# Kernel optimization log

Measured on AMD Instinct MI355X. Metric: run time of the kernel, lower is better.

## Reference

```python
import jax, jax.numpy as jnp
import numpy as np

MA_K = 2 * 125 + 1  # 251, moving-average kernel
MV_K = 4 * 125 + 1  # 501, moving-variance kernel
EPS = 1e-5


def _avg_pool1d(x, K):
    """PyTorch F.avg_pool1d(stride=1, padding=(K-1)//2, count_include_pad=True)
    computed in O(L) via prefix sums. x: (B, C, L) -> (B, C, L)."""
    pad = (K - 1) // 2
    xp = jnp.pad(x, ((0, 0), (0, 0), (pad, pad)))  # zero pad, length L+K-1
    c = jnp.pad(jnp.cumsum(xp, axis=-1), ((0, 0), (0, 0), (1, 0)))  # length L+K
    return (c[..., K:] - c[..., :-K]) / K  # divide by K always (count_include_pad)


def setup_inputs() -> dict:
    key = jax.random.key(0)
    x = jax.random.normal(key, (8192, 1, 3750), dtype=jnp.float32)
    return {"x": x}


def reference(x):
    # global z-norm per (batch, channel); torch.std is unbiased (ddof=1)
    x = (x - jnp.mean(x, axis=2, keepdims=True)) / (
        jnp.std(x, axis=2, keepdims=True, ddof=1) + EPS)
    # remove moving average (kernel 251)
    x = x - _avg_pool1d(x, MA_K)
    # rescale by moving std (kernel 501)
    x = x / (jnp.sqrt(_avg_pool1d(x * x, MV_K)) + EPS)
    return x
```

## Files before the change

### kernel.cpp

```cpp
#include <hip/hip_runtime.h>
#include <math.h>

namespace {

constexpr int L      = 3750;
constexpr int NPAIR  = L / 2;
constexpr int BLK    = 256;
constexpr int CH     = 15;
constexpr int NCHUNK = L / CH;
constexpr int NFULL  = NPAIR / BLK;
constexpr int NTAIL  = NPAIR - NFULL * BLK;
constexpr float EPS  = 1e-5f;

__device__ __forceinline__ float frcp(float x)  { return __builtin_amdgcn_rcpf(x); }
__device__ __forceinline__ float fsqrt(float x) { return __builtin_amdgcn_sqrtf(x); }
__device__ __forceinline__ float frsq(float x)  { return __builtin_amdgcn_rsqf(x); }

__global__ __launch_bounds__(BLK, 8)
void preproc_kernel(const float* __restrict__ in, float* __restrict__ out) {
    __shared__ __align__(16) float sp[L + 2];
    __shared__ float sred[8];

    const int tid  = threadIdx.x;
    const int lane = tid & 63;
    const int wave = tid >> 6;
    const size_t rowoff = (size_t)blockIdx.x * (size_t)L;
    const float* rin  = in  + rowoff;
    float*       rout = out + rowoff;

    const bool active = (tid < NCHUNK);
    const int  base   = tid * CH;
    const bool tl     = (tid < NTAIL);

    {
        const float2* rin2 = reinterpret_cast<const float2*>(rin);
        float2 v[NFULL + 1];
        #pragma unroll
        for (int k = 0; k < NFULL; ++k) v[k] = rin2[k * BLK + tid];
        if (tl) v[NFULL] = rin2[NFULL * BLK + tid];
        float2* sp2 = reinterpret_cast<float2*>(sp);
        #pragma unroll
        for (int k = 0; k < NFULL; ++k) sp2[k * BLK + tid] = v[k];
        if (tl) sp2[NFULL * BLK + tid] = v[NFULL];
    }
    __syncthreads();

    float y[CH];
    float cy = 0.f, cy2 = 0.f;
    if (active) {
        #pragma unroll
        for (int j = 0; j < CH; ++j) {
            const float v = sp[base + j];
            y[j] = v;
            cy  += v;
            cy2  = fmaf(v, v, cy2);
        }
    } else {
        #pragma unroll
        for (int j = 0; j < CH; ++j) y[j] = 0.f;
    }
    float iy = cy;
    #pragma unroll
    for (int d = 1; d < 64; d <<= 1) {
        const float u = __shfl_up(iy, (unsigned)d, 64);
        if (lane >= d) iy += u;
    }
    float t2 = cy2;
    #pragma unroll
    for (int d = 1; d < 64; d <<= 1) t2 += __shfl_xor(t2, d, 64);
    if (lane == 63) { sred[wave] = iy; sred[4 + wave] = t2; }
    __syncthreads();
    float woff = 0.f;
    #pragma unroll
    for (int w = 0; w < 4; ++w) if (w < wave) woff += sred[w];
    const float totY  = sred[0] + sred[1] + sred[2] + sred[3];
    const float totY2 = sred[4] + sred[5] + sred[6] + sred[7];
    const float mean  = totY * (1.f / (float)L);
    const float var   = (totY2 - totY * mean) * (1.f / (float)(L - 1));
    const float s     = fsqrt(var) + EPS;
    const float epsS  = EPS * s;

    {
        float run = woff + iy - cy;
        if (active) {
            #pragma unroll
            for (int j = 0; j < CH; ++j) { sp[base + j] = run; run += y[j]; }
            if (tid == NCHUNK - 1) sp[L] = run;
        }
    }
    __syncthreads();

    const float inv251 = 1.f / 251.f;
    float cu = 0.f;
    if (active) {
        if (tid >= 9 && tid <= 240) {
            #pragma unroll
            for (int j = 0; j < CH; ++j) {
                const int i = base + j;
                const float sumY = sp[i + 126] - sp[i - 125];
                const float u = fmaf(sumY, -inv251, y[j]);
                y[j] = u;
                cu   = fmaf(u, u, cu);
            }
        } else {
            #pragma unroll
            for (int j = 0; j < CH; ++j) {
                const int i  = base + j;
                const int lo = (i > 125) ? i - 125 : 0;
                const int hi = (i + 126 < L) ? i + 126 : L;
                const float sumY = sp[hi] - sp[lo];
                const float cnt  = (float)(hi - lo);
                float u = y[j] - mean * (1.f - cnt * inv251);
                u = fmaf(sumY, -inv251, u);
                y[j] = u;
                cu   = fmaf(u, u, cu);
            }
        }
    }
    float iu = cu;
    #pragma unroll
    for (int d = 1; d < 64; d <<= 1) {
        const float u = __shfl_up(iu, (unsigned)d, 64);
        if (lane >= d) iu += u;
    }
    if (lane == 63) sred[wave] = iu;
    __syncthreads();
    float woff2 = 0.f;
    #pragma unroll
    for (int w = 0; w < 4; ++w) if (w < wave) woff2 += sred[w];

    {
        float run = woff2 + iu - cu;
        if (active) {
            #pragma unroll
            for (int j = 0; j < CH; ++j) { sp[base + j] = run; run = fmaf(y[j], y[j], run); }
            if (tid == NCHUNK - 1) sp[L] = run;
        }
    }
    __syncthreads();

    const float inv501 = 1.f / 501.f;
    if (active) {
        if (tid >= 17 && tid <= 232) {
            #pragma unroll
            for (int j = 0; j < CH; ++j) {
                const int i = base + j;
                const float W = fmaxf((sp[i + 251] - sp[i - 250]) * inv501, 0.f);
                const float t = frsq(W);
                y[j] = y[j] * t * fmaf(-epsS, t, 1.f);
            }
        } else {
            #pragma unroll
            for (int j = 0; j < CH; ++j) {
                const int i  = base + j;
                const int lo = (i > 250) ? i - 250 : 0;
                const int hi = (i + 251 < L) ? i + 251 : L;
                const float W = fmaxf((sp[hi] - sp[lo]) * inv501, 0.f);
                const float t = frsq(W);
                y[j] = y[j] * t * fmaf(-epsS, t, 1.f);
            }
        }
    }
    __syncthreads();

    if (active) {
        #pragma unroll
        for (int j = 0; j < CH; ++j) sp[base + j] = y[j];
    }
    __syncthreads();

    {
        const float2* sp2 = reinterpret_cast<const float2*>(sp);
        float2* rout2 = reinterpret_cast<float2*>(rout);
        float2 v[NFULL + 1];
        #pragma unroll
        for (int k = 0; k < NFULL; ++k) v[k] = sp2[k * BLK + tid];
        if (tl) v[NFULL] = sp2[NFULL * BLK + tid];
        #pragma unroll
        for (int k = 0; k < NFULL; ++k) rout2[k * BLK + tid] = v[k];
        if (tl) rout2[NFULL * BLK + tid] = v[NFULL];
    }
}

}

extern "C" void kernel_launch(void* const* d_in, const int* in_sizes, int n_in,
                              void* d_out, int out_size, void* d_ws, size_t ws_size,
                              hipStream_t stream) {
    const float* x = (const float*)d_in[0];
    float* out = (float*)d_out;
    const int rows = in_sizes[0] / L;
    preproc_kernel<<<rows, BLK, 0, stream>>>(x, out);
}
```

Measured before the change: 44.61 us.

## Process two rows per block to amortize barriers and raise per-thread ILP

Each block now handles two rows at once, interleaving the scans, reductions and window passes for both rows between shared barriers. This halves the number of barriers and launches per row and gives each thread independent work to overlap latency. The cost is doubled LDS per block and more registers (launch bounds lowered from 8 to 5), which reduces how many blocks fit per CU, and it assumes an even row count.

```diff
diff --git a/kernel.cpp b/kernel.cpp
--- a/kernel.cpp
+++ b/kernel.cpp
@@ -6,6 +6,7 @@
 constexpr int L      = 3750;
 constexpr int NPAIR  = L / 2;
 constexpr int BLK    = 256;
+constexpr int ROWS   = 2;
 constexpr int CH     = 15;
 constexpr int NCHUNK = L / CH;
 constexpr int NFULL  = NPAIR / BLK;
@@ -16,169 +17,206 @@
 __device__ __forceinline__ float fsqrt(float x) { return __builtin_amdgcn_sqrtf(x); }
 __device__ __forceinline__ float frsq(float x)  { return __builtin_amdgcn_rsqf(x); }
 
-__global__ __launch_bounds__(BLK, 8)
+__global__ __launch_bounds__(BLK, 5)
 void preproc_kernel(const float* __restrict__ in, float* __restrict__ out) {
-    __shared__ __align__(16) float sp[L + 2];
-    __shared__ float sred[8];
+    __shared__ __align__(16) float sp[ROWS][L + 2];
+    __shared__ float sred[ROWS][8];
 
     const int tid  = threadIdx.x;
     const int lane = tid & 63;
     const int wave = tid >> 6;
-    const size_t rowoff = (size_t)blockIdx.x * (size_t)L;
-    const float* rin  = in  + rowoff;
-    float*       rout = out + rowoff;
+    const size_t row0 = (size_t)blockIdx.x * (size_t)ROWS;
 
     const bool active = (tid < NCHUNK);
     const int  base   = tid * CH;
     const bool tl     = (tid < NTAIL);
 
     {
-        const float2* rin2 = reinterpret_cast<const float2*>(rin);
-        float2 v[NFULL + 1];
-        #pragma unroll
-        for (int k = 0; k < NFULL; ++k) v[k] = rin2[k * BLK + tid];
-        if (tl) v[NFULL] = rin2[NFULL * BLK + tid];
-        float2* sp2 = reinterpret_cast<float2*>(sp);
-        #pragma unroll
-        for (int k = 0; k < NFULL; ++k) sp2[k * BLK + tid] = v[k];
-        if (tl) sp2[NFULL * BLK + tid] = v[NFULL];
-    }
-    __syncthreads();
-
-    float y[CH];
-    float cy = 0.f, cy2 = 0.f;
-    if (active) {
-        #pragma unroll
-        for (int j = 0; j < CH; ++j) {
-            const float v = sp[base + j];
-            y[j] = v;
-            cy  += v;
-            cy2  = fmaf(v, v, cy2);
-        }
-    } else {
-        #pragma unroll
-        for (int j = 0; j < CH; ++j) y[j] = 0.f;
-    }
-    float iy = cy;
-    #pragma unroll
-    for (int d = 1; d < 64; d <<= 1) {
-        const float u = __shfl_up(iy, (unsigned)d, 64);
-        if (lane >= d) iy += u;
-    }
-    float t2 = cy2;
-    #pragma unroll
-    for (int d = 1; d < 64; d <<= 1) t2 += __shfl_xor(t2, d, 64);
-    if (lane == 63) { sred[wave] = iy; sred[4 + wave] = t2; }
-    __syncthreads();
-    float woff = 0.f;
-    #pragma unroll
-    for (int w = 0; w < 4; ++w) if (w < wave) woff += sred[w];
-    const float totY  = sred[0] + sred[1] + sred[2] + sred[3];
-    const float totY2 = sred[4] + sred[5] + sred[6] + sred[7];
-    const float mean  = totY * (1.f / (float)L);
-    const float var   = (totY2 - totY * mean) * (1.f / (float)(L - 1));
-    const float s     = fsqrt(var) + EPS;
-    const float epsS  = EPS * s;
+        float2 v[ROWS][NFULL + 1];
+        #pragma unroll
+        for (int r = 0; r < ROWS; ++r) {
+            const float2* rin2 = reinterpret_cast<const float2*>(in + (row0 + r) * L);
+            #pragma unroll
+            for (int k = 0; k < NFULL; ++k) v[r][k] = rin2[k * BLK + tid];
+            if (tl) v[r][NFULL] = rin2[NFULL * BLK + tid];
+        }
+        #pragma unroll
+        for (int r = 0; r < ROWS; ++r) {
+            float2* sp2 = reinterpret_cast<float2*>(&sp[r][0]);
+            #pragma unroll
+            for (int k = 0; k < NFULL; ++k) sp2[k * BLK + tid] = v[r][k];
+            if (tl) sp2[NFULL * BLK + tid] = v[r][NFULL];
+        }
+    }
+    __syncthreads();
+
+    float y[ROWS][CH];
+    float cy[ROWS], iy[ROWS];
+    #pragma unroll
+    for (int r = 0; r < ROWS; ++r) {
+        float c = 0.f, c2 = 0.f;
+        if (active) {
+            #pragma unroll
+            for (int j = 0; j < CH; ++j) {
+                const float v = sp[r][base + j];
+                y[r][j] = v;
+                c  += v;
+                c2  = fmaf(v, v, c2);
+            }
+        } else {
+            #pragma unroll
+            for (int j = 0; j < CH; ++j) y[r][j] = 0.f;
+        }
+        float i1 = c;
+        #pragma unroll
+        for (int d = 1; d < 64; d <<= 1) {
+            const float u = __shfl_up(i1, (unsigned)d, 64);
+            if (lane >= d) i1 += u;
+        }
+        float t2 = c2;
+        #pragma unroll
+        for (int d = 1; d < 64; d <<= 1) t2 += __shfl_xor(t2, d, 64);
+        if (lane == 63) { sred[r][wave] = i1; sred[r][4 + wave] = t2; }
+        cy[r] = c; iy[r] = i1;
+    }
+    __syncthreads();
+
+    float mean[ROWS], epsS[ROWS], woff[ROWS];
+    #pragma unroll
+    for (int r = 0; r < ROWS; ++r) {
+        float wo = 0.f;
+        #pragma unroll
+        for (int w = 0; w < 4; ++w) if (w < wave) wo += sred[r][w];
+        woff[r] = wo;
+        const float totY  = sred[r][0] + sred[r][1] + sred[r][2] + sred[r][3];
+        const float totY2 = sred[r][4] + sred[r][5] + sred[r][6] + sred[r][7];
+        mean[r] = totY * (1.f / (float)L);
+        const float var = (totY2 - totY * mean[r]) * (1.f / (float)(L - 1));
+        const float s   = fsqrt(var) + EPS;
+        epsS[r] = EPS * s;
+    }
+
+    #pragma unroll
+    for (int r = 0; r < ROWS; ++r) {
+        if (active) {
+            float run = woff[r] + iy[r] - cy[r];
+            #pragma unroll
+            for (int j = 0; j < CH; ++j) { sp[r][base + j] = run; run += y[r][j]; }
+            if (tid == NCHUNK - 1) sp[r][L] = run;
+        }
+    }
+    __syncthreads();
+
+    const float inv251 = 1.f / 251.f;
+    float cu[ROWS], iu[ROWS];
+    #pragma unroll
+    for (int r = 0; r < ROWS; ++r) {
+        float c = 0.f;
+        if (active) {
+            if (tid >= 9 && tid <= 240) {
+                #pragma unroll
+                for (int j = 0; j < CH; ++j) {
+                    const int i = base + j;
+                    const float sumY = sp[r][i + 126] - sp[r][i - 125];
+                    const float u = fmaf(sumY, -inv251, y[r][j]);
+                    y[r][j] = u;
+                    c = fmaf(u, u, c);
+                }
+            } else {
+                #pragma unroll
+                for (int j = 0; j < CH; ++j) {
+                    const int i  = base + j;
+                    const int lo = (i > 125) ? i - 125 : 0;
+                    const int hi = (i + 126 < L) ? i + 126 : L;
+                    const float sumY = sp[r][hi] - sp[r][lo];
+                    const float cnt  = (float)(hi - lo);
+                    float u = y[r][j] - mean[r] * (1.f - cnt * inv251);
+                    u = fmaf(sumY, -inv251, u);
+                    y[r][j] = u;
+                    c = fmaf(u, u, c);
+                }
+            }
+        }
+        float i1 = c;
+        #pragma unroll
+        for (int d = 1; d < 64; d <<= 1) {
+            const float u = __shfl_up(i1, (unsigned)d, 64);
+            if (lane >= d) i1 += u;
+        }
+        if (lane == 63) sred[r][wave] = i1;
+        cu[r] = c; iu[r] = i1;
+    }
+    __syncthreads();
+
+    #pragma unroll
+    for (int r = 0; r < ROWS; ++r) {
+        if (active) {
+            float wo = 0.f;
+            #pragma unroll
+            for (int w = 0; w < 4; ++w) if (w < wave) wo += sred[r][w];
+            float run = wo + iu[r] - cu[r];
+            #pragma unroll
+            for (int j = 0; j < CH; ++j) {
+                sp[r][base + j] = run;
+                run = fmaf(y[r][j], y[r][j], run);
+            }
+            if (tid == NCHUNK - 1) sp[r][L] = run;
+        }
+    }
+    __syncthreads();
+
+    const float inv501 = 1.f / 501.f;
+    #pragma unroll
+    for (int r = 0; r < ROWS; ++r) {
+        if (active) {
+            if (tid >= 17 && tid <= 232) {
+                #pragma unroll
+                for (int j = 0; j < CH; ++j) {
+                    const int i = base + j;
+                    const float W = fmaxf((sp[r][i + 251] - sp[r][i - 250]) * inv501, 0.f);
+                    const float t = frsq(W);
+                    y[r][j] = y[r][j] * t * fmaf(-epsS[r], t, 1.f);
+                }
+            } else {
+                #pragma unroll
+                for (int j = 0; j < CH; ++j) {
+                    const int i  = base + j;
+                    const int lo = (i > 250) ? i - 250 : 0;
+                    const int hi = (i + 251 < L) ? i + 251 : L;
+                    const float W = fmaxf((sp[r][hi] - sp[r][lo]) * inv501, 0.f);
+                    const float t = frsq(W);
+                    y[r][j] = y[r][j] * t * fmaf(-epsS[r], t, 1.f);
+                }
+            }
+        }
+    }
+    __syncthreads();
+
+    #pragma unroll
+    for (int r = 0; r < ROWS; ++r) {
+        if (active) {
+            #pragma unroll
+            for (int j = 0; j < CH; ++j) sp[r][base + j] = y[r][j];
+        }
+    }
+    __syncthreads();
 
     {
-        float run = woff + iy - cy;
-        if (active) {
-            #pragma unroll
-            for (int j = 0; j < CH; ++j) { sp[base + j] = run; run += y[j]; }
-            if (tid == NCHUNK - 1) sp[L] = run;
-        }
-    }
-    __syncthreads();
-
-    const float inv251 = 1.f / 251.f;
-    float cu = 0.f;
-    if (active) {
-        if (tid >= 9 && tid <= 240) {
-            #pragma unroll
-            for (int j = 0; j < CH; ++j) {
-                const int i = base + j;
-                const float sumY = sp[i + 126] - sp[i - 125];
-                const float u = fmaf(sumY, -inv251, y[j]);
-                y[j] = u;
-                cu   = fmaf(u, u, cu);
-            }
-        } else {
-            #pragma unroll
-            for (int j = 0; j < CH; ++j) {
-                const int i  = base + j;
-                const int lo = (i > 125) ? i - 125 : 0;
-                const int hi = (i + 126 < L) ? i + 126 : L;
-                const float sumY = sp[hi] - sp[lo];
-                const float cnt  = (float)(hi - lo);
-                float u = y[j] - mean * (1.f - cnt * inv251);
-                u = fmaf(sumY, -inv251, u);
-                y[j] = u;
-                cu   = fmaf(u, u, cu);
-            }
-        }
-    }
-    float iu = cu;
-    #pragma unroll
-    for (int d = 1; d < 64; d <<= 1) {
-        const float u = __shfl_up(iu, (unsigned)d, 64);
-        if (lane >= d) iu += u;
-    }
-    if (lane == 63) sred[wave] = iu;
-    __syncthreads();
-    float woff2 = 0.f;
-    #pragma unroll
-    for (int w = 0; w < 4; ++w) if (w < wave) woff2 += sred[w];
-
-    {
-        float run = woff2 + iu - cu;
-        if (active) {
-            #pragma unroll
-            for (int j = 0; j < CH; ++j) { sp[base + j] = run; run = fmaf(y[j], y[j], run); }
-            if (tid == NCHUNK - 1) sp[L] = run;
-        }
-    }
-    __syncthreads();
-
-    const float inv501 = 1.f / 501.f;
-    if (active) {
-        if (tid >= 17 && tid <= 232) {
-            #pragma unroll
-            for (int j = 0; j < CH; ++j) {
-                const int i = base + j;
-                const float W = fmaxf((sp[i + 251] - sp[i - 250]) * inv501, 0.f);
-                const float t = frsq(W);
-                y[j] = y[j] * t * fmaf(-epsS, t, 1.f);
-            }
-        } else {
-            #pragma unroll
-            for (int j = 0; j < CH; ++j) {
-                const int i  = base + j;
-                const int lo = (i > 250) ? i - 250 : 0;
-                const int hi = (i + 251 < L) ? i + 251 : L;
-                const float W = fmaxf((sp[hi] - sp[lo]) * inv501, 0.f);
-                const float t = frsq(W);
-                y[j] = y[j] * t * fmaf(-epsS, t, 1.f);
-            }
-        }
-    }
-    __syncthreads();
-
-    if (active) {
-        #pragma unroll
-        for (int j = 0; j < CH; ++j) sp[base + j] = y[j];
-    }
-    __syncthreads();
-
-    {
-        const float2* sp2 = reinterpret_cast<const float2*>(sp);
-        float2* rout2 = reinterpret_cast<float2*>(rout);
-        float2 v[NFULL + 1];
-        #pragma unroll
-        for (int k = 0; k < NFULL; ++k) v[k] = sp2[k * BLK + tid];
-        if (tl) v[NFULL] = sp2[NFULL * BLK + tid];
-        #pragma unroll
-        for (int k = 0; k < NFULL; ++k) rout2[k * BLK + tid] = v[k];
-        if (tl) rout2[NFULL * BLK + tid] = v[NFULL];
+        float2 v[ROWS][NFULL + 1];
+        #pragma unroll
+        for (int r = 0; r < ROWS; ++r) {
+            const float2* sp2 = reinterpret_cast<const float2*>(&sp[r][0]);
+            #pragma unroll
+            for (int k = 0; k < NFULL; ++k) v[r][k] = sp2[k * BLK + tid];
+            if (tl) v[r][NFULL] = sp2[NFULL * BLK + tid];
+        }
+        #pragma unroll
+        for (int r = 0; r < ROWS; ++r) {
+            float2* rout2 = reinterpret_cast<float2*>(out + (row0 + r) * L);
+            #pragma unroll
+            for (int k = 0; k < NFULL; ++k) rout2[k * BLK + tid] = v[r][k];
+            if (tl) rout2[NFULL * BLK + tid] = v[r][NFULL];
+        }
     }
 }
 
@@ -190,5 +228,5 @@
     const float* x = (const float*)d_in[0];
     float* out = (float*)d_out;
     const int rows = in_sizes[0] / L;
-    preproc_kernel<<<rows, BLK, 0, stream>>>(x, out);
+    preproc_kernel<<<rows / ROWS, BLK, 0, stream>>>(x, out);
 }
```

New measurement: 49.53 us. +11.0%, slower.
